# Kernel tuning notes

Measured on AMD Instinct MI355X. Metric: run time of the kernel, lower is better.

## Reference

```python
import jax, jax.numpy as jnp
import numpy as np

WS, OWS, NHEAD = 4, 6, 6          # window, overlap window = 4 + int(0.5*4), heads
B, CIN, COU, H, W = 2, 192, 192, 224, 224
MID = CIN  # r = 1


def calc_rpi_oca(ws=WS, ows=OWS):
    # relative position index between ws x ws query window and ows x ows overlapping kv window
    co = np.stack(np.meshgrid(np.arange(ws), np.arange(ws), indexing='ij')).reshape(2, -1)
    ce = np.stack(np.meshgrid(np.arange(ows), np.arange(ows), indexing='ij')).reshape(2, -1)
    rel = (ce[:, None, :] - co[:, :, None]).transpose(1, 2, 0) + (ws - 1)  # [ws*ws, ows*ows, 2], >= 0
    idx = rel[..., 0] * (ws + ows - 1) + rel[..., 1]                       # in [0, (ws+ows-1)^2)
    return jnp.asarray(idx)  # [16, 36]

RPI = calc_rpi_oca()


def conv2d(x, w, b, pad):
    out = jax.lax.conv_general_dilated(x, w, (1, 1), [(pad, pad), (pad, pad)],
                                       dimension_numbers=('NCHW', 'OIHW', 'NCHW'))
    return out + b[None, :, None, None]


def group_norm(x, g, b, groups, eps=1e-5):
    n = x.shape[0]
    xg = x.reshape(n, groups, -1)
    mu = xg.mean(-1, keepdims=True)
    var = xg.var(-1, keepdims=True)
    xn = ((xg - mu) * jax.lax.rsqrt(var + eps)).reshape(x.shape)
    return xn * g[None, :, None, None] + b[None, :, None, None]


def layer_norm(x, g, b, eps=1e-5):
    mu = x.mean(-1, keepdims=True)
    var = x.var(-1, keepdims=True)
    return (x - mu) * jax.lax.rsqrt(var + eps) * g + b


def ocab(x, h, w, ln1_g, ln1_b, qkv_w, qkv_b, rpb, proj_w, proj_b,
         ln2_g, ln2_b, fc1_w, fc1_b, fc2_w, fc2_b):
    b, _, c = x.shape
    nh, nw, d = h // WS, w // WS, c // NHEAD
    shortcut = x
    xn = layer_norm(x, ln1_g, ln1_b).reshape(b, h, w, c)
    qkv = xn @ qkv_w + qkv_b                                  # [b,h,w,3c] laid out [q|k|v]
    q = qkv[..., :c]
    kv = jnp.stack([qkv[..., c:2 * c], qkv[..., 2 * c:]])     # [2,b,h,w,c]
    # non-overlapping query windows -> [b*nwin, 16, NHEAD, d]
    qw = q.reshape(b, nh, WS, nw, WS, c).transpose(0, 1, 3, 2, 4, 5).reshape(b * nh * nw, WS * WS, NHEAD, d)
    # overlapping kv windows = Unfold(kernel=OWS, stride=WS, pad=(OWS-WS)//2)
    pad = (OWS - WS) // 2
    kvp = jnp.pad(kv, ((0, 0), (0, 0), (pad, pad), (pad, pad), (0, 0)))
    rows = (jnp.arange(nh) * WS)[:, None] + jnp.arange(OWS)[None, :]   # [nh, OWS]
    cols = (jnp.arange(nw) * WS)[:, None] + jnp.arange(OWS)[None, :]   # [nw, OWS]
    patches = kvp[:, :, rows[:, None, :, None], cols[None, :, None, :], :]  # [2,b,nh,nw,OWS,OWS,c]
    kvw = patches.reshape(2, b * nh * nw, OWS * OWS, NHEAD, d)
    kw, vw = kvw[0], kvw[1]
    attn = jnp.einsum('wqhd,wkhd->whqk', qw * (d ** -0.5), kw)  # [b*nwin, NHEAD, 16, 36]
    bias = rpb[RPI.reshape(-1)].reshape(WS * WS, OWS * OWS, NHEAD).transpose(2, 0, 1)
    attn = jax.nn.softmax(attn + bias[None], axis=-1)
    out = jnp.einsum('whqk,wkhd->wqhd', attn, vw).reshape(b, nh, nw, WS, WS, c)
    out = out.transpose(0, 1, 3, 2, 4, 5).reshape(b, h * w, c)  # window_reverse
    out = out @ proj_w + proj_b + shortcut
    xm = layer_norm(out, ln2_g, ln2_b)
    mlp = jax.nn.gelu(xm @ fc1_w + fc1_b, approximate=False) @ fc2_w + fc2_b
    return out + mlp


def atoca_forward(x, conv1_w, conv1_b, gn1_g, gn1_b, conv2_w, conv2_b, gn2_g, gn2_b,
                  conv3_w, conv3_b, ln1_g, ln1_b, qkv_w, qkv_b, rpb, proj_w, proj_b,
                  ln2_g, ln2_b, fc1_w, fc1_b, fc2_w, fc2_b):
    Bx, C, Hx, Wx = x.shape
    shortcut = x
    # raw row-major reshape, exactly as the torch code (not a spatial window partition)
    out = x.reshape(Bx * (Hx // WS) * (Wx // WS), C, WS, WS)
    out = conv2d(out, conv1_w, conv1_b, 1)
    out = jax.nn.silu(group_norm(out, gn1_g, gn1_b, NHEAD))
    out = out.transpose(0, 2, 3, 1).reshape(Bx, Hx * Wx, -1)
    out = ocab(out, Hx, Wx, ln1_g, ln1_b, qkv_w, qkv_b, rpb, proj_w, proj_b,
               ln2_g, ln2_b, fc1_w, fc1_b, fc2_w, fc2_b)
    out = out.reshape(Bx * (Hx // WS) * (Wx // WS), WS, WS, -1).transpose(0, 3, 1, 2)
    out = conv2d(out, conv2_w, conv2_b, 1)
    out = group_norm(out, gn2_g, gn2_b, NHEAD)
    out = out.reshape(Bx, -1, Hx, Wx)
    out = out + conv2d(shortcut, conv3_w, conv3_b, 0)
    return jax.nn.relu(out)


def setup_inputs() -> dict:
    key = jax.random.key(0)
    ks = iter(jax.random.split(key, 32))
    rn = lambda shape, s=0.02: (s * jax.random.normal(next(ks), shape)).astype(jnp.float32)
    return {
        'x': jax.random.normal(next(ks), (B, CIN, H, W), dtype=jnp.float32),
        'conv1_w': rn((MID, CIN, 3, 3)), 'conv1_b': rn((MID,)),
        'gn1_g': jnp.ones((MID,), jnp.float32), 'gn1_b': jnp.zeros((MID,), jnp.float32),
        'conv2_w': rn((COU, MID, 3, 3)), 'conv2_b': rn((COU,)),
        'gn2_g': jnp.ones((COU,), jnp.float32), 'gn2_b': jnp.zeros((COU,), jnp.float32),
        'conv3_w': rn((COU, CIN, 1, 1)), 'conv3_b': rn((COU,)),
        'ln1_g': jnp.ones((MID,), jnp.float32), 'ln1_b': jnp.zeros((MID,), jnp.float32),
        'qkv_w': rn((MID, 3 * MID)), 'qkv_b': rn((3 * MID,)),
        'rpb': rn(((WS + OWS - 1) ** 2, NHEAD)),
        'proj_w': rn((MID, MID)), 'proj_b': rn((MID,)),
        'ln2_g': jnp.ones((MID,), jnp.float32), 'ln2_b': jnp.zeros((MID,), jnp.float32),
        'fc1_w': rn((MID, 2 * MID)), 'fc1_b': rn((2 * MID,)),
        'fc2_w': rn((2 * MID, MID)), 'fc2_b': rn((MID,)),
    }


def reference(x, conv1_w, conv1_b, gn1_g, gn1_b, conv2_w, conv2_b, gn2_g, gn2_b,
              conv3_w, conv3_b, ln1_g, ln1_b, qkv_w, qkv_b, rpb, proj_w, proj_b,
              ln2_g, ln2_b, fc1_w, fc1_b, fc2_w, fc2_b):
    return atoca_forward(x, conv1_w, conv1_b, gn1_g, gn1_b, conv2_w, conv2_b, gn2_g, gn2_b,
                         conv3_w, conv3_b, ln1_g, ln1_b, qkv_w, qkv_b, rpb, proj_w, proj_b,
                         ln2_g, ln2_b, fc1_w, fc1_b, fc2_w, fc2_b)
```

## Files before the change

### kernel.cpp

```cpp
#include <hip/hip_runtime.h>
#include <hip/hip_bf16.h>
#include <math.h>

typedef __hip_bfloat16 bf16;
typedef __attribute__((ext_vector_type(8))) short s8v;
typedef __attribute__((ext_vector_type(4))) short s4v;
typedef __attribute__((ext_vector_type(4))) float f32x4;
typedef __attribute__((ext_vector_type(2))) _Float16 h2;

constexpr int CB   = 2;
constexpr int CH   = 224, CW = 224;
constexpr int NHW  = 56;
constexpr int NPATCH = CB * NHW * NHW;
constexpr int TOKPB  = CH * CW;
constexpr int MTOK   = CB * TOKPB;
constexpr size_t SECSZ = 19267584;

constexpr size_t B_T0  = 0;
constexpr size_t B_P2  = B_T0 + 38535168;
constexpr size_t B_P3  = B_P2 + 115605504;
constexpr size_t B_P4  = B_P3 + 38535168;
constexpr size_t B_WF1 = B_P4 + 38535168;
constexpr size_t B_WF2 = B_WF1 + 1327104;
constexpr size_t B_W3F = B_WF2 + 1327104;
constexpr size_t B_WQ  = B_W3F + 147456;
constexpr size_t B_WP  = B_WQ + 221184;
constexpr size_t B_WG1 = B_WP + 73728;
constexpr size_t B_WG2 = B_WG1 + 147456;
constexpr size_t WS_NEEDED = B_WG2 + 147456;

__device__ __forceinline__ float ldf(const float* p) { return *p; }
__device__ __forceinline__ float ldf(const bf16* p)  { return __bfloat162float(*p); }
__device__ __forceinline__ void  stf(float* p, float v) { *p = v; }
__device__ __forceinline__ void  stf(bf16* p, float v)  { *p = __float2bfloat16(v); }
__device__ __forceinline__ unsigned short f2bf(float f) {
    unsigned u = __builtin_bit_cast(unsigned, f);
    unsigned r = (u + 0x7fffu + ((u >> 16) & 1u)) >> 16;
    return (unsigned short)r;
}
__device__ __forceinline__ float bf2f(short s) {
    unsigned u = ((unsigned)(unsigned short)s) << 16;
    return __builtin_bit_cast(float, u);
}

__device__ __forceinline__ void prep_wf(const float* __restrict__ w, short* __restrict__ wf, int o) {
    int within = o & 511, frag = o >> 9;
    int l = within >> 3, j = within & 7;
    int nt = frag % 12, t2 = frag / 12, ks = t2 % 6, tap = t2 / 6;
    int co = nt * 16 + (l & 15);
    int ci = ks * 32 + (l >> 4) * 8 + j;
    wf[o] = (short)f2bf(w[(co * 192 + ci) * 9 + tap]);
}
__device__ __forceinline__ void prep_wgemm(const float* __restrict__ w, short* __restrict__ wf,
                                           int K, int N, int o) {
    int j = o & 7, l = (o >> 3) & 63, f = o >> 9;
    int ntiles = N >> 4;
    int kt = f / ntiles, nt = f % ntiles;
    int k = kt * 32 + (l >> 4) * 8 + j;
    int col = nt * 16 + (l & 15);
    wf[o] = (short)f2bf(w[(size_t)k * N + col]);
}
__device__ __forceinline__ void prep_w3f(const float* __restrict__ w, short* __restrict__ wf, int o) {
    int j = o & 7, l = (o >> 3) & 63, f = o >> 9;
    int kt = f / 12, ct = f % 12;
    int co = ct * 16 + (l & 15);
    int ci = kt * 32 + (l >> 4) * 8 + j;
    wf[o] = (short)f2bf(w[co * 192 + ci]);
}
__global__ __launch_bounds__(256) void prep_all_kernel(
    const float* __restrict__ conv1_w, short* __restrict__ WF1,
    const float* __restrict__ conv2_w, short* __restrict__ WF2,
    const float* __restrict__ conv3_w, short* __restrict__ W3F,
    const float* __restrict__ qkv_w,   short* __restrict__ WQ,
    const float* __restrict__ proj_w,  short* __restrict__ WP,
    const float* __restrict__ fc1_w,   short* __restrict__ WG1,
    const float* __restrict__ fc2_w,   short* __restrict__ WG2)
{
    int o = blockIdx.x * 256 + threadIdx.x;
    if (o < 331776)            { prep_wf(conv1_w, WF1, o); return; }
    o -= 331776;
    if (o < 331776)            { prep_wf(conv2_w, WF2, o); return; }
    o -= 331776;
    if (o < 36864)             { prep_w3f(conv3_w, W3F, o); return; }
    o -= 36864;
    if (o < 110592)            { prep_wgemm(qkv_w, WQ, 192, 576, o); return; }
    o -= 110592;
    if (o < 36864)             { prep_wgemm(proj_w, WP, 192, 192, o); return; }
    o -= 36864;
    if (o < 73728)             { prep_wgemm(fc1_w, WG1, 192, 384, o); return; }
    o -= 73728;
    if (o < 73728)             { prep_wgemm(fc2_w, WG2, 384, 192, o); return; }
}
constexpr int PREP_TOTAL = 331776 * 2 + 36864 + 110592 + 36864 + 73728 * 2;

template <bool FIRST>
__global__ __launch_bounds__(256, 4) void conv_mfma_kernel(
    const void* __restrict__ srcv, const short* __restrict__ wf,
    const float* __restrict__ bias, const float* __restrict__ gng,
    const float* __restrict__ gnb, bf16* __restrict__ dst)
{
    __shared__ short xs[13056];
    __shared__ float gsum[4][6], gsum2[4][6], gmu[4][6], grs[4][6];
    const int tid  = threadIdx.x;
    const int lane = tid & 63, wid = tid >> 6;
    const int n0   = blockIdx.x * 4;

    if (tid < 24) { gsum[tid / 6][tid % 6] = 0.f; gsum2[tid / 6][tid % 6] = 0.f; }
    for (int u = tid; u < 4 * 192; u += 256) {
        int q = u / 192;
        xs[q * 3264 + 3072 + (u % 192)] = 0;
    }

    if constexpr (FIRST) {
        const float4* sp = (const float4*)((const float*)srcv + (size_t)n0 * 3072);
        #pragma unroll
        for (int u = 0; u < 12; ++u) {
            int idx = u * 256 + tid;
            float4 v = sp[idx];
            int q = idx / 768;
            int li = (idx % 768) * 4;
            int ci = li >> 4, p0 = li & 15;
            float vv[4] = { v.x, v.y, v.z, v.w };
            #pragma unroll
            for (int k = 0; k < 4; ++k) {
                int row = p0 + k;
                int ba = q * 6528 + ((row * 384 + ci * 2) ^ ((row & 7) << 4));
                *(short*)((char*)xs + ba) = (short)f2bf(vv[k]);
            }
        }
    } else {
        const s8v* sp8 = (const s8v*)((const bf16*)srcv + (size_t)n0 * 3072);
        #pragma unroll
        for (int u = 0; u < 6; ++u) {
            int li = u * 256 + tid;
            int r = li / 24, ch = li % 24;
            int q = r >> 4, rl = r & 15;
            s8v val = sp8[li];
            int ba = q * 6528 + ((rl * 384 + ch * 16) ^ ((rl & 7) << 4));
            *(s8v*)((char*)xs + ba) = val;
        }
    }
    __syncthreads();

    const int ntb = wid * 3;
    const int cl  = lane & 15;
    const int kg  = lane >> 4;
    f32x4 acc[3][4];
    #pragma unroll
    for (int t = 0; t < 3; ++t) {
        float bv = bias[(ntb + t) * 16 + cl];
        #pragma unroll
        for (int q = 0; q < 4; ++q) acc[t][q] = (f32x4){ bv, bv, bv, bv };
    }

    const int pi = cl >> 2, pj = cl & 3;
    const s8v* wf8 = (const s8v*)wf;

    for (int tap = 0; tap < 9; ++tap) {
        const int di = tap / 3, dj = tap % 3;
        const int ii = pi + di - 1, jj = pj + dj - 1;
        const bool valid = (ii >= 0 && ii < 4 && jj >= 0 && jj < 4);
        const int nr  = valid ? (ii * 4 + jj) : 16;
        const int rb  = nr * 384;
        const int swz = (nr & 7) << 4;
        #pragma unroll
        for (int ks = 0; ks < 6; ++ks) {
            const s8v* bp = wf8 + (size_t)((tap * 6 + ks) * 12) * 64 + lane;
            s8v b0 = bp[(ntb + 0) * 64];
            s8v b1 = bp[(ntb + 1) * 64];
            s8v b2 = bp[(ntb + 2) * 64];
            const int inner = (rb + ks * 64 + kg * 16) ^ swz;
            #pragma unroll
            for (int q = 0; q < 4; ++q) {
                s8v a = *(const s8v*)((const char*)xs + q * 6528 + inner);
                acc[0][q] = __builtin_amdgcn_mfma_f32_16x16x32_bf16(a, b0, acc[0][q], 0, 0, 0);
                acc[1][q] = __builtin_amdgcn_mfma_f32_16x16x32_bf16(a, b1, acc[1][q], 0, 0, 0);
                acc[2][q] = __builtin_amdgcn_mfma_f32_16x16x32_bf16(a, b2, acc[2][q], 0, 0, 0);
            }
        }
    }

    #pragma unroll
    for (int t = 0; t < 3; ++t) {
        const int g = (ntb + t) >> 1;
        #pragma unroll
        for (int q = 0; q < 4; ++q) {
            f32x4 A = acc[t][q];
            float s  = A[0] + A[1] + A[2] + A[3];
            float s2 = A[0]*A[0] + A[1]*A[1] + A[2]*A[2] + A[3]*A[3];
            #pragma unroll
            for (int off = 32; off; off >>= 1) { s += __shfl_xor(s, off); s2 += __shfl_xor(s2, off); }
            if (lane == 0) { atomicAdd(&gsum[q][g], s); atomicAdd(&gsum2[q][g], s2); }
        }
    }
    __syncthreads();
    if (tid < 24) {
        int q = tid / 6, g = tid % 6;
        float mu  = gsum[q][g] * (1.f / 512.f);
        float var = gsum2[q][g] * (1.f / 512.f) - mu * mu;
        gmu[q][g] = mu; grs[q][g] = rsqrtf(var + 1e-5f);
    }
    __syncthreads();

    if constexpr (FIRST) {
        #pragma unroll
        for (int t = 0; t < 3; ++t) {
            const int co = (ntb + t) * 16 + cl, g = (ntb + t) >> 1;
            const float gg = gng[co], gb = gnb[co];
            #pragma unroll
            for (int q = 0; q < 4; ++q) {
                const float mu = gmu[q][g], rs = grs[q][g];
                #pragma unroll
                for (int r = 0; r < 4; ++r) {
                    float v = (acc[t][q][r] - mu) * rs * gg + gb;
                    v = v / (1.f + __expf(-v));
                    int row = q * 16 + kg * 4 + r;
                    int ba = (row * 384 + co * 2) ^ ((row & 7) << 4);
                    *(short*)((char*)xs + ba) = (short)f2bf(v);
                }
            }
        }
        __syncthreads();
        bf16* dp = dst + (size_t)n0 * 3072;
        #pragma unroll
        for (int u = 0; u < 6; ++u) {
            int li = u * 256 + tid;
            int row = li / 24, g2 = li % 24;
            int ba = (row * 384 + g2 * 16) ^ ((row & 7) << 4);
            s8v val = *(const s8v*)((const char*)xs + ba);
            *(s8v*)(dp + (size_t)row * 192 + g2 * 8) = val;
        }
    } else {
        #pragma unroll
        for (int t = 0; t < 3; ++t) {
            const int co = (ntb + t) * 16 + cl, g = (ntb + t) >> 1;
            const float gg = gng[co], gb = gnb[co];
            #pragma unroll
            for (int q = 0; q < 4; ++q) {
                const float mu = gmu[q][g], rs = grs[q][g];
                #pragma unroll
                for (int r = 0; r < 4; ++r) {
                    float v = (acc[t][q][r] - mu) * rs * gg + gb;
                    xs[q * 3072 + co * 16 + kg * 4 + r] = (short)f2bf(v);
                }
            }
        }
        __syncthreads();
        s4v* dp = (s4v*)(dst + (size_t)n0 * 3072);
        const s4v* sps = (const s4v*)xs;
        #pragma unroll
        for (int u = 0; u < 12; ++u) {
            dp[u * 256 + tid] = sps[u * 256 + tid];
        }
    }
}

template <bool RES, bool GELU_ACT, bool LN, bool QKVOUT, int NKT>
__global__ __launch_bounds__(256) void gemm_mfma_kernel(
    const bf16* __restrict__ A, const short* __restrict__ wfb,
    const float* __restrict__ bias, const bf16* __restrict__ res,
    void* __restrict__ out, int N,
    const float* __restrict__ lng, const float* __restrict__ lnb)
{
    __shared__ short ls[8192];
    const int tid = threadIdx.x, lane = tid & 63, wid = tid >> 6;
    const int m0 = blockIdx.x * 128;
    const int cl = lane & 15, kg = lane >> 4;
    constexpr int K = NKT * 32;
    const int ntiles = N >> 4;
    const int ntsec = ntiles / gridDim.y;
    const int ntbeg = blockIdx.y * ntsec;

    s8v af0[NKT], af1[NKT];
    const int r0 = m0 + wid * 32 + cl;
    #pragma unroll
    for (int kt = 0; kt < NKT; ++kt) {
        af0[kt] = *(const s8v*)(A + (size_t)r0 * K + kt * 32 + kg * 8);
        af1[kt] = *(const s8v*)(A + (size_t)(r0 + 16) * K + kt * 32 + kg * 8);
    }
    if constexpr (LN) {
        static_assert(!LN || NKT == 6, "LN requires K==192");
        #pragma unroll
        for (int r = 0; r < 2; ++r) {
            s8v* af = r ? af1 : af0;
            float s = 0.f, s2 = 0.f;
            #pragma unroll
            for (int kt = 0; kt < NKT; ++kt)
                #pragma unroll
                for (int j = 0; j < 8; ++j) {
                    float v = bf2f(af[kt][j]);
                    s += v; s2 += v * v;
                }
            s  += __shfl_xor(s, 16);  s2 += __shfl_xor(s2, 16);
            s  += __shfl_xor(s, 32);  s2 += __shfl_xor(s2, 32);
            const float mu = s * (1.f / 192.f);
            const float rs = rsqrtf(s2 * (1.f / 192.f) - mu * mu + 1e-5f);
            #pragma unroll
            for (int kt = 0; kt < NKT; ++kt) {
                const float* gp = lng + kt * 32 + kg * 8;
                const float* bp = lnb + kt * 32 + kg * 8;
                #pragma unroll
                for (int j = 0; j < 8; ++j) {
                    float v = (bf2f(af[kt][j]) - mu) * rs * gp[j] + bp[j];
                    af[kt][j] = (short)f2bf(v);
                }
            }
        }
    }

    const s8v* wf8 = (const s8v*)wfb;
    for (int nt0 = ntbeg; nt0 < ntbeg + ntsec; nt0 += 4) {
        const int n0 = nt0 * 16;
        f32x4 acc[2][4];
        #pragma unroll
        for (int nf = 0; nf < 4; ++nf) {
            float bv = bias[n0 + nf * 16 + cl];
            acc[0][nf] = (f32x4){ bv, bv, bv, bv };
            acc[1][nf] = (f32x4){ bv, bv, bv, bv };
        }
        #pragma unroll
        for (int kt = 0; kt < NKT; ++kt) {
            #pragma unroll
            for (int nf = 0; nf < 4; ++nf) {
                s8v b = wf8[(size_t)(kt * ntiles + nt0 + nf) * 64 + lane];
                acc[0][nf] = __builtin_amdgcn_mfma_f32_16x16x32_bf16(af0[kt], b, acc[0][nf], 0, 0, 0);
                acc[1][nf] = __builtin_amdgcn_mfma_f32_16x16x32_bf16(af1[kt], b, acc[1][nf], 0, 0, 0);
            }
        }

        __syncthreads();
        #pragma unroll
        for (int rf = 0; rf < 2; ++rf) {
            #pragma unroll
            for (int nf = 0; nf < 4; ++nf) {
                const int lcol = nf * 16 + cl;
                #pragma unroll
                for (int r = 0; r < 4; ++r) {
                    const int lrow = wid * 32 + rf * 16 + kg * 4 + r;
                    float v = acc[rf][nf][r];
                    if (GELU_ACT) v = 0.5f * v * (1.f + erff(v * 0.70710678118f));
                    short sv;
                    if constexpr (QKVOUT) sv = __builtin_bit_cast(short, (_Float16)v);
                    else                  sv = (short)f2bf(v);
                    int ba = (lrow * 128 + lcol * 2) ^ ((lrow & 7) << 4);
                    *(short*)((char*)ls + ba) = sv;
                }
            }
        }
        __syncthreads();
        #pragma unroll
        for (int p = 0; p < 4; ++p) {
            const int lrow = p * 32 + (tid >> 3);
            const int g = tid & 7;
            int ba = (lrow * 128 + g * 16) ^ ((lrow & 7) << 4);
            s8v val = *(const s8v*)((const char*)ls + ba);
            const int row = m0 + lrow;
            const int col0 = n0 + g * 8;
            if constexpr (QKVOUT) {
                const int sec = n0 / 192;
                const int c0 = col0 - sec * 192, h = c0 >> 5, d0 = c0 & 31;
                const int bb2 = row / TOKPB, t = row - bb2 * TOKPB;
                *(s8v*)((_Float16*)out + (size_t)sec * SECSZ +
                        ((size_t)(bb2 * 6 + h) * TOKPB + t) * 32 + d0) = val;
            } else if constexpr (RES) {
                s8v rv = *(const s8v*)(res + (size_t)row * N + col0);
                s8v ov;
                #pragma unroll
                for (int e = 0; e < 8; ++e) ov[e] = (short)f2bf(bf2f(val[e]) + bf2f(rv[e]));
                *(s8v*)((bf16*)out + (size_t)row * N + col0) = ov;
            } else {
                *(s8v*)((bf16*)out + (size_t)row * N + col0) = val;
            }
        }
    }
}

constexpr int HSTR = 1160;
__global__ __launch_bounds__(128) void attn_proj_kernel(
    const _Float16* __restrict__ qf, const float* __restrict__ rpb,
    const short* __restrict__ wpf, const float* __restrict__ pb,
    const bf16* __restrict__ t0, bf16* __restrict__ omid)
{
    __shared__ __align__(16) short kh[6 * HSTR];
    __shared__ __align__(16) short vh[6 * HSTR];
    const int w = blockIdx.x;
    const int b = w / (NHW * NHW), wi = w % (NHW * NHW);
    const int nhi = wi / NHW, nwi = wi % NHW;
    const int tid = threadIdx.x;
    const int lane = tid & 63, wid = tid >> 6;
    const int r0 = nhi * 4 - 1, c0 = nwi * 4 - 1;
    const _Float16* kfb = qf + SECSZ;
    const _Float16* vfb = qf + 2 * SECSZ;

    #pragma unroll
    for (int it = 0; it < 14; ++it) {
        int v = tid + it * 128;
        if (v < 1728) {
            int kv = v >= 864 ? 1 : 0;
            int u = v - kv * 864;
            int h = u / 144, rem = u % 144, kj = rem >> 2, d0 = (rem & 3) * 8;
            int rr = r0 + kj / 6, cc = c0 + kj % 6;
            s8v val = { 0, 0, 0, 0, 0, 0, 0, 0 };
            if (rr >= 0 && rr < CH && cc >= 0 && cc < CW) {
                const _Float16* src = kv ? vfb : kfb;
                val = *(const s8v*)(src + ((size_t)(b * 6 + h) * TOKPB + rr * CW + cc) * 32 + d0);
            }
            short* dst = kv ? vh : kh;
            *(s8v*)(dst + h * HSTR + kj * 32 + d0) = val;
        }
    }
    __syncthreads();

    h2 o2[16];
    float inv = 0.f;
    if (tid < 96) {
        const int h = tid >> 4, qi = tid & 15;
        const int qr = nhi * 4 + (qi >> 2), qc = nwi * 4 + (qi & 3);
        const _Float16* qp = qf + ((size_t)(b * 6 + h) * TOKPB + qr * CW + qc) * 32;
        h2 qh[16];
        #pragma unroll
        for (int u = 0; u < 4; ++u) {
            uint4 qa = *(const uint4*)(qp + u * 8);
            qh[u * 4 + 0] = __builtin_bit_cast(h2, qa.x);
            qh[u * 4 + 1] = __builtin_bit_cast(h2, qa.y);
            qh[u * 4 + 2] = __builtin_bit_cast(h2, qa.z);
            qh[u * 4 + 3] = __builtin_bit_cast(h2, qa.w);
        }

        float sc[36];
        const short* khb = kh + h * HSTR;
        #pragma unroll
        for (int kj = 0; kj < 36; ++kj) {
            const uint4* kp = (const uint4*)(khb + kj * 32);
            uint4 k0 = kp[0], k1 = kp[1], k2 = kp[2], k3 = kp[3];
            unsigned kwv[16] = { k0.x, k0.y, k0.z, k0.w, k1.x, k1.y, k1.z, k1.w,
                                 k2.x, k2.y, k2.z, k2.w, k3.x, k3.y, k3.z, k3.w };
            float a0 = 0.f, a1 = 0.f, a2 = 0.f, a3 = 0.f;
            #pragma unroll
            for (int e = 0; e < 4; ++e) {
                a0 = __builtin_amdgcn_fdot2(__builtin_bit_cast(h2, kwv[4*e+0]), qh[4*e+0], a0, false);
                a1 = __builtin_amdgcn_fdot2(__builtin_bit_cast(h2, kwv[4*e+1]), qh[4*e+1], a1, false);
                a2 = __builtin_amdgcn_fdot2(__builtin_bit_cast(h2, kwv[4*e+2]), qh[4*e+2], a2, false);
                a3 = __builtin_amdgcn_fdot2(__builtin_bit_cast(h2, kwv[4*e+3]), qh[4*e+3], a3, false);
            }
            const int rel0 = kj / 6 - (qi >> 2) + 3;
            const int rel1 = kj % 6 - (qi & 3) + 3;
            sc[kj] = ((a0 + a1) + (a2 + a3)) * 0.17677669529f + rpb[(rel0 * 9 + rel1) * 6 + h];
        }
        float mx = -1e30f;
        #pragma unroll
        for (int kj = 0; kj < 36; ++kj) mx = fmaxf(mx, sc[kj]);
        float sum = 0.f;
        #pragma unroll
        for (int kj = 0; kj < 36; ++kj) { sc[kj] = __expf(sc[kj] - mx); sum += sc[kj]; }
        inv = 1.f / sum;

        #pragma unroll
        for (int e = 0; e < 16; ++e) o2[e] = (h2){ (_Float16)0.f, (_Float16)0.f };
        const short* vhb = vh + h * HSTR;
        #pragma unroll
        for (int kj = 0; kj < 36; ++kj) {
            const uint4* vp = (const uint4*)(vhb + kj * 32);
            uint4 v0 = vp[0], v1 = vp[1], v2 = vp[2], v3 = vp[3];
            unsigned vwv[16] = { v0.x, v0.y, v0.z, v0.w, v1.x, v1.y, v1.z, v1.w,
                                 v2.x, v2.y, v2.z, v2.w, v3.x, v3.y, v3.z, v3.w };
            const _Float16 ph = (_Float16)sc[kj];
            const h2 ph2 = { ph, ph };
            #pragma unroll
            for (int e = 0; e < 16; ++e)
                o2[e] = __builtin_bit_cast(h2, vwv[e]) * ph2 + o2[e];
        }
    }
    __syncthreads();

    if (tid < 96) {
        const int h = tid >> 4, qi = tid & 15;
        #pragma unroll
        for (int u = 0; u < 4; ++u) {
            s8v pk;
            #pragma unroll
            for (int e = 0; e < 4; ++e) {
                h2 ov = o2[u * 4 + e];
                pk[2 * e]     = (short)f2bf((float)ov[0] * inv);
                pk[2 * e + 1] = (short)f2bf((float)ov[1] * inv);
            }
            int ba = (qi * 384 + (h * 32 + u * 8) * 2) ^ ((qi & 7) << 4);
            *(s8v*)((char*)kh + ba) = pk;
        }
    }
    __syncthreads();

    const int cl = lane & 15, kg = lane >> 4;
    s8v a[6];
    #pragma unroll
    for (int kt = 0; kt < 6; ++kt) {
        int ba = (cl * 384 + kt * 64 + kg * 16) ^ ((cl & 7) << 4);
        a[kt] = *(const s8v*)((const char*)kh + ba);
    }
    f32x4 acc[6];
    const s8v* wp8 = (const s8v*)wpf;
    #pragma unroll
    for (int ctl = 0; ctl < 6; ++ctl) {
        float bv = pb[(wid * 6 + ctl) * 16 + cl];
        acc[ctl] = (f32x4){ bv, bv, bv, bv };
    }
    #pragma unroll
    for (int kt = 0; kt < 6; ++kt) {
        #pragma unroll
        for (int ctl = 0; ctl < 6; ++ctl) {
            s8v bfr = wp8[(size_t)(kt * 12 + wid * 6 + ctl) * 64 + lane];
            acc[ctl] = __builtin_amdgcn_mfma_f32_16x16x32_bf16(a[kt], bfr, acc[ctl], 0, 0, 0);
        }
    }
    #pragma unroll
    for (int ctl = 0; ctl < 6; ++ctl) {
        const int col = (wid * 6 + ctl) * 16 + cl;
        #pragma unroll
        for (int r = 0; r < 4; ++r) {
            vh[(kg * 4 + r) * 192 + col] = (short)f2bf(acc[ctl][r]);
        }
    }
    __syncthreads();

    #pragma unroll
    for (int u = 0; u < 3; ++u) {
        int li = u * 128 + tid;
        int row = li / 24, c8 = (li % 24) * 8;
        int qr = nhi * 4 + (row >> 2), qc = nwi * 4 + (row & 3);
        size_t gb = ((size_t)(b * TOKPB + qr * CW + qc)) * 192 + c8;
        s8v pv = *(const s8v*)(vh + row * 192 + c8);
        s8v rv = *(const s8v*)(t0 + gb);
        s8v ov;
        #pragma unroll
        for (int e = 0; e < 8; ++e) ov[e] = (short)f2bf(bf2f(pv[e]) + bf2f(rv[e]));
        *(s8v*)(omid + gb) = ov;
    }
}

__global__ __launch_bounds__(256, 4) void final_mfma_kernel(
    const float* __restrict__ x, const short* __restrict__ w3f,
    const float* __restrict__ b3, const bf16* __restrict__ c2,
    float* __restrict__ out)
{
    __shared__ short xs2[12288];
    const int pix0 = blockIdx.x * 64;
    const int b    = blockIdx.y;
    const int tid = threadIdx.x, lane = tid & 63, wid = tid >> 6;
    const int cl = lane & 15, kg = lane >> 4;
    const float* xb = x + (size_t)b * (192 * TOKPB);

    #pragma unroll
    for (int u = 0; u < 12; ++u) {
        int idx = u * 256 + tid;
        int ci = idx >> 4, p4 = (idx & 15) << 2;
        float4 v = *(const float4*)(xb + (size_t)ci * TOKPB + pix0 + p4);
        float vv[4] = { v.x, v.y, v.z, v.w };
        #pragma unroll
        for (int k = 0; k < 4; ++k) {
            int row = p4 + k;
            int ba = (row * 384 + ci * 2) ^ ((row & 7) << 4);
            *(short*)((char*)xs2 + ba) = (short)f2bf(vv[k]);
        }
    }
    __syncthreads();

    const int ctb = wid * 3;
    f32x4 acc[3][4] = {};
    const s8v* wf8 = (const s8v*)w3f;

    #pragma unroll
    for (int kt = 0; kt < 6; ++kt) {
        s8v a0 = wf8[(size_t)(kt * 12 + ctb + 0) * 64 + lane];
        s8v a1 = wf8[(size_t)(kt * 12 + ctb + 1) * 64 + lane];
        s8v a2 = wf8[(size_t)(kt * 12 + ctb + 2) * 64 + lane];
        #pragma unroll
        for (int pt = 0; pt < 4; ++pt) {
            int row = pt * 16 + cl;
            int ba = (row * 384 + kt * 64 + kg * 16) ^ ((row & 7) << 4);
            s8v bfr = *(const s8v*)((const char*)xs2 + ba);
            acc[0][pt] = __builtin_amdgcn_mfma_f32_16x16x32_bf16(a0, bfr, acc[0][pt], 0, 0, 0);
            acc[1][pt] = __builtin_amdgcn_mfma_f32_16x16x32_bf16(a1, bfr, acc[1][pt], 0, 0, 0);
            acc[2][pt] = __builtin_amdgcn_mfma_f32_16x16x32_bf16(a2, bfr, acc[2][pt], 0, 0, 0);
        }
    }

    #pragma unroll
    for (int t = 0; t < 3; ++t) {
        #pragma unroll
        for (int r = 0; r < 4; ++r) {
            const int co = (ctb + t) * 16 + kg * 4 + r;
            const float bb = b3[co];
            const size_t rowbase = (size_t)b * (192 * TOKPB) + (size_t)co * TOKPB + pix0;
            #pragma unroll
            for (int pt = 0; pt < 4; ++pt) {
                const size_t f = rowbase + pt * 16 + cl;
                float v = acc[t][pt][r] + bb + bf2f(__builtin_bit_cast(short, c2[f]));
                out[f] = fmaxf(v, 0.f);
            }
        }
    }
}

extern "C" void kernel_launch(void* const* d_in, const int* in_sizes, int n_in,
                              void* d_out, int out_size, void* d_ws, size_t ws_size,
                              hipStream_t stream)
{
    if (ws_size < WS_NEEDED) return;

    const float* x       = (const float*)d_in[0];
    const float* conv1_w = (const float*)d_in[1];
    const float* conv1_b = (const float*)d_in[2];
    const float* gn1_g   = (const float*)d_in[3];
    const float* gn1_b   = (const float*)d_in[4];
    const float* conv2_w = (const float*)d_in[5];
    const float* conv2_b = (const float*)d_in[6];
    const float* gn2_g   = (const float*)d_in[7];
    const float* gn2_b   = (const float*)d_in[8];
    const float* conv3_w = (const float*)d_in[9];
    const float* conv3_b = (const float*)d_in[10];
    const float* ln1_g   = (const float*)d_in[11];
    const float* ln1_b   = (const float*)d_in[12];
    const float* qkv_w   = (const float*)d_in[13];
    const float* qkv_b   = (const float*)d_in[14];
    const float* rpb     = (const float*)d_in[15];
    const float* proj_w  = (const float*)d_in[16];
    const float* proj_b  = (const float*)d_in[17];
    const float* ln2_g   = (const float*)d_in[18];
    const float* ln2_b   = (const float*)d_in[19];
    const float* fc1_w   = (const float*)d_in[20];
    const float* fc1_b   = (const float*)d_in[21];
    const float* fc2_w   = (const float*)d_in[22];
    const float* fc2_b   = (const float*)d_in[23];

    char* wsb = (char*)d_ws;
    bf16*  T0  = (bf16*)(wsb + B_T0);
    _Float16* QF = (_Float16*)(wsb + B_P2);
    bf16*  HID = (bf16*)(wsb + B_P2);
    bf16*  P3  = (bf16*)(wsb + B_P3);
    bf16*  P4  = (bf16*)(wsb + B_P4);
    short* WF1 = (short*)(wsb + B_WF1);
    short* WF2 = (short*)(wsb + B_WF2);
    short* W3F = (short*)(wsb + B_W3F);
    short* WQ  = (short*)(wsb + B_WQ);
    short* WP  = (short*)(wsb + B_WP);
    short* WG1 = (short*)(wsb + B_WG1);
    short* WG2 = (short*)(wsb + B_WG2);
    float* OUT = (float*)d_out;

    prep_all_kernel<<<(PREP_TOTAL + 255) / 256, 256, 0, stream>>>(
        conv1_w, WF1, conv2_w, WF2, conv3_w, W3F, qkv_w, WQ, proj_w, WP, fc1_w, WG1, fc2_w, WG2);

    conv_mfma_kernel<true><<<NPATCH / 4, 256, 0, stream>>>(x, WF1, conv1_b, gn1_g, gn1_b, T0);
    gemm_mfma_kernel<false, false, true, true, 6><<<dim3(MTOK / 128, 1), 256, 0, stream>>>(
        T0, WQ, qkv_b, nullptr, QF, 576, ln1_g, ln1_b);
    attn_proj_kernel<<<NPATCH, 128, 0, stream>>>(QF, rpb, WP, proj_b, T0, P4);
    gemm_mfma_kernel<false, true, true, false, 6><<<dim3(MTOK / 128, 1), 256, 0, stream>>>(
        P4, WG1, fc1_b, nullptr, HID, 384, ln2_g, ln2_b);
    gemm_mfma_kernel<true, false, false, false, 12><<<dim3(MTOK / 128, 1), 256, 0, stream>>>(
        HID, WG2, fc2_b, P4, P3, 192, nullptr, nullptr);
    conv_mfma_kernel<false><<<NPATCH / 4, 256, 0, stream>>>(P3, WF2, conv2_b, gn2_g, gn2_b, P4);
    final_mfma_kernel<<<dim3(TOKPB / 64, CB), 256, 0, stream>>>(x, W3F, conv3_b, P4, OUT);
}
```

Before: 525.6 us.

## Split attention keys across thread pairs and widen attn block to three waves

After: 506.9 us (median of 3 runs). -3.6%, faster.

```diff
diff --git a/kernel.cpp b/kernel.cpp
--- a/kernel.cpp
+++ b/kernel.cpp
@@ -376,7 +376,7 @@
 }
 
 constexpr int HSTR = 1160;
-__global__ __launch_bounds__(128) void attn_proj_kernel(
+__global__ __launch_bounds__(192) void attn_proj_kernel(
     const _Float16* __restrict__ qf, const float* __restrict__ rpb,
     const short* __restrict__ wpf, const float* __restrict__ pb,
     const bf16* __restrict__ t0, bf16* __restrict__ omid)
@@ -393,88 +393,93 @@
     const _Float16* vfb = qf + 2 * SECSZ;
 
     #pragma unroll
-    for (int it = 0; it < 14; ++it) {
-        int v = tid + it * 128;
-        if (v < 1728) {
-            int kv = v >= 864 ? 1 : 0;
-            int u = v - kv * 864;
-            int h = u / 144, rem = u % 144, kj = rem >> 2, d0 = (rem & 3) * 8;
-            int rr = r0 + kj / 6, cc = c0 + kj % 6;
-            s8v val = { 0, 0, 0, 0, 0, 0, 0, 0 };
-            if (rr >= 0 && rr < CH && cc >= 0 && cc < CW) {
-                const _Float16* src = kv ? vfb : kfb;
-                val = *(const s8v*)(src + ((size_t)(b * 6 + h) * TOKPB + rr * CW + cc) * 32 + d0);
-            }
-            short* dst = kv ? vh : kh;
-            *(s8v*)(dst + h * HSTR + kj * 32 + d0) = val;
-        }
-    }
-    __syncthreads();
+    for (int it = 0; it < 9; ++it) {
+        int v = tid + it * 192;
+        int kv = v >= 864 ? 1 : 0;
+        int u = v - kv * 864;
+        int h = u / 144, rem = u % 144, kj = rem >> 2, d0 = (rem & 3) * 8;
+        int rr = r0 + kj / 6, cc = c0 + kj % 6;
+        s8v val = { 0, 0, 0, 0, 0, 0, 0, 0 };
+        if (rr >= 0 && rr < CH && cc >= 0 && cc < CW) {
+            const _Float16* src = kv ? vfb : kfb;
+            val = *(const s8v*)(src + ((size_t)(b * 6 + h) * TOKPB + rr * CW + cc) * 32 + d0);
+        }
+        short* dst = kv ? vh : kh;
+        *(s8v*)(dst + h * HSTR + kj * 32 + d0) = val;
+    }
+    __syncthreads();
+
+    const int pair = tid >> 1, split = tid & 1;
+    const int h = pair >> 4, qi = pair & 15;
+    const int qr = nhi * 4 + (qi >> 2), qc = nwi * 4 + (qi & 3);
+    const _Float16* qp = qf + ((size_t)(b * 6 + h) * TOKPB + qr * CW + qc) * 32;
+    h2 qh[16];
+    #pragma unroll
+    for (int u = 0; u < 4; ++u) {
+        uint4 qa = *(const uint4*)(qp + u * 8);
+        qh[u * 4 + 0] = __builtin_bit_cast(h2, qa.x);
+        qh[u * 4 + 1] = __builtin_bit_cast(h2, qa.y);
+        qh[u * 4 + 2] = __builtin_bit_cast(h2, qa.z);
+        qh[u * 4 + 3] = __builtin_bit_cast(h2, qa.w);
+    }
+
+    float sc[18];
+    const int kbeg = split * 18;
+    const short* khb = kh + h * HSTR;
+    #pragma unroll
+    for (int kk = 0; kk < 18; ++kk) {
+        const int kj = kbeg + kk;
+        const uint4* kp = (const uint4*)(khb + kj * 32);
+        uint4 k0 = kp[0], k1 = kp[1], k2 = kp[2], k3 = kp[3];
+        unsigned kwv[16] = { k0.x, k0.y, k0.z, k0.w, k1.x, k1.y, k1.z, k1.w,
+                             k2.x, k2.y, k2.z, k2.w, k3.x, k3.y, k3.z, k3.w };
+        float a0 = 0.f, a1 = 0.f, a2 = 0.f, a3 = 0.f;
+        #pragma unroll
+        for (int e = 0; e < 4; ++e) {
+            a0 = __builtin_amdgcn_fdot2(__builtin_bit_cast(h2, kwv[4*e+0]), qh[4*e+0], a0, false);
+            a1 = __builtin_amdgcn_fdot2(__builtin_bit_cast(h2, kwv[4*e+1]), qh[4*e+1], a1, false);
+            a2 = __builtin_amdgcn_fdot2(__builtin_bit_cast(h2, kwv[4*e+2]), qh[4*e+2], a2, false);
+            a3 = __builtin_amdgcn_fdot2(__builtin_bit_cast(h2, kwv[4*e+3]), qh[4*e+3], a3, false);
+        }
+        const int rel0 = kj / 6 - (qi >> 2) + 3;
+        const int rel1 = kj % 6 - (qi & 3) + 3;
+        sc[kk] = ((a0 + a1) + (a2 + a3)) * 0.17677669529f + rpb[(rel0 * 9 + rel1) * 6 + h];
+    }
+    float mx = -1e30f;
+    #pragma unroll
+    for (int kk = 0; kk < 18; ++kk) mx = fmaxf(mx, sc[kk]);
+    mx = fmaxf(mx, __shfl_xor(mx, 1));
+    float sum = 0.f;
+    #pragma unroll
+    for (int kk = 0; kk < 18; ++kk) { sc[kk] = __expf(sc[kk] - mx); sum += sc[kk]; }
+    sum += __shfl_xor(sum, 1);
+    const float inv = 1.f / sum;
 
     h2 o2[16];
-    float inv = 0.f;
-    if (tid < 96) {
-        const int h = tid >> 4, qi = tid & 15;
-        const int qr = nhi * 4 + (qi >> 2), qc = nwi * 4 + (qi & 3);
-        const _Float16* qp = qf + ((size_t)(b * 6 + h) * TOKPB + qr * CW + qc) * 32;
-        h2 qh[16];
-        #pragma unroll
-        for (int u = 0; u < 4; ++u) {
-            uint4 qa = *(const uint4*)(qp + u * 8);
-            qh[u * 4 + 0] = __builtin_bit_cast(h2, qa.x);
-            qh[u * 4 + 1] = __builtin_bit_cast(h2, qa.y);
-            qh[u * 4 + 2] = __builtin_bit_cast(h2, qa.z);
-            qh[u * 4 + 3] = __builtin_bit_cast(h2, qa.w);
-        }
-
-        float sc[36];
-        const short* khb = kh + h * HSTR;
-        #pragma unroll
-        for (int kj = 0; kj < 36; ++kj) {
-            const uint4* kp = (const uint4*)(khb + kj * 32);
-            uint4 k0 = kp[0], k1 = kp[1], k2 = kp[2], k3 = kp[3];
-            unsigned kwv[16] = { k0.x, k0.y, k0.z, k0.w, k1.x, k1.y, k1.z, k1.w,
-                                 k2.x, k2.y, k2.z, k2.w, k3.x, k3.y, k3.z, k3.w };
-            float a0 = 0.f, a1 = 0.f, a2 = 0.f, a3 = 0.f;
-            #pragma unroll
-            for (int e = 0; e < 4; ++e) {
-                a0 = __builtin_amdgcn_fdot2(__builtin_bit_cast(h2, kwv[4*e+0]), qh[4*e+0], a0, false);
-                a1 = __builtin_amdgcn_fdot2(__builtin_bit_cast(h2, kwv[4*e+1]), qh[4*e+1], a1, false);
-                a2 = __builtin_amdgcn_fdot2(__builtin_bit_cast(h2, kwv[4*e+2]), qh[4*e+2], a2, false);
-                a3 = __builtin_amdgcn_fdot2(__builtin_bit_cast(h2, kwv[4*e+3]), qh[4*e+3], a3, false);
-            }
-            const int rel0 = kj / 6 - (qi >> 2) + 3;
-            const int rel1 = kj % 6 - (qi & 3) + 3;
-            sc[kj] = ((a0 + a1) + (a2 + a3)) * 0.17677669529f + rpb[(rel0 * 9 + rel1) * 6 + h];
-        }
-        float mx = -1e30f;
-        #pragma unroll
-        for (int kj = 0; kj < 36; ++kj) mx = fmaxf(mx, sc[kj]);
-        float sum = 0.f;
-        #pragma unroll
-        for (int kj = 0; kj < 36; ++kj) { sc[kj] = __expf(sc[kj] - mx); sum += sc[kj]; }
-        inv = 1.f / sum;
-
-        #pragma unroll
-        for (int e = 0; e < 16; ++e) o2[e] = (h2){ (_Float16)0.f, (_Float16)0.f };
-        const short* vhb = vh + h * HSTR;
-        #pragma unroll
-        for (int kj = 0; kj < 36; ++kj) {
-            const uint4* vp = (const uint4*)(vhb + kj * 32);
-            uint4 v0 = vp[0], v1 = vp[1], v2 = vp[2], v3 = vp[3];
-            unsigned vwv[16] = { v0.x, v0.y, v0.z, v0.w, v1.x, v1.y, v1.z, v1.w,
-                                 v2.x, v2.y, v2.z, v2.w, v3.x, v3.y, v3.z, v3.w };
-            const _Float16 ph = (_Float16)sc[kj];
-            const h2 ph2 = { ph, ph };
-            #pragma unroll
-            for (int e = 0; e < 16; ++e)
-                o2[e] = __builtin_bit_cast(h2, vwv[e]) * ph2 + o2[e];
-        }
-    }
-    __syncthreads();
-
-    if (tid < 96) {
-        const int h = tid >> 4, qi = tid & 15;
+    #pragma unroll
+    for (int e = 0; e < 16; ++e) o2[e] = (h2){ (_Float16)0.f, (_Float16)0.f };
+    const short* vhb = vh + h * HSTR;
+    #pragma unroll
+    for (int kk = 0; kk < 18; ++kk) {
+        const int kj = kbeg + kk;
+        const uint4* vp = (const uint4*)(vhb + kj * 32);
+        uint4 v0 = vp[0], v1 = vp[1], v2 = vp[2], v3 = vp[3];
+        unsigned vwv[16] = { v0.x, v0.y, v0.z, v0.w, v1.x, v1.y, v1.z, v1.w,
+                             v2.x, v2.y, v2.z, v2.w, v3.x, v3.y, v3.z, v3.w };
+        const _Float16 ph = (_Float16)sc[kk];
+        const h2 ph2 = { ph, ph };
+        #pragma unroll
+        for (int e = 0; e < 16; ++e)
+            o2[e] = __builtin_bit_cast(h2, vwv[e]) * ph2 + o2[e];
+    }
+    #pragma unroll
+    for (int e = 0; e < 16; ++e) {
+        unsigned other = __shfl_xor(__builtin_bit_cast(unsigned, o2[e]), 1);
+        o2[e] = o2[e] + __builtin_bit_cast(h2, other);
+    }
+    __syncthreads();
+
+    if (split == 0) {
         #pragma unroll
         for (int u = 0; u < 4; ++u) {
             s8v pk;
@@ -497,24 +502,24 @@
         int ba = (cl * 384 + kt * 64 + kg * 16) ^ ((cl & 7) << 4);
         a[kt] = *(const s8v*)((const char*)kh + ba);
     }
-    f32x4 acc[6];
+    f32x4 acc[4];
     const s8v* wp8 = (const s8v*)wpf;
     #pragma unroll
-    for (int ctl = 0; ctl < 6; ++ctl) {
-        float bv = pb[(wid * 6 + ctl) * 16 + cl];
+    for (int ctl = 0; ctl < 4; ++ctl) {
+        float bv = pb[(wid * 4 + ctl) * 16 + cl];
         acc[ctl] = (f32x4){ bv, bv, bv, bv };
     }
     #pragma unroll
     for (int kt = 0; kt < 6; ++kt) {
         #pragma unroll
-        for (int ctl = 0; ctl < 6; ++ctl) {
-            s8v bfr = wp8[(size_t)(kt * 12 + wid * 6 + ctl) * 64 + lane];
+        for (int ctl = 0; ctl < 4; ++ctl) {
+            s8v bfr = wp8[(size_t)(kt * 12 + wid * 4 + ctl) * 64 + lane];
             acc[ctl] = __builtin_amdgcn_mfma_f32_16x16x32_bf16(a[kt], bfr, acc[ctl], 0, 0, 0);
         }
     }
     #pragma unroll
-    for (int ctl = 0; ctl < 6; ++ctl) {
-        const int col = (wid * 6 + ctl) * 16 + cl;
+    for (int ctl = 0; ctl < 4; ++ctl) {
+        const int col = (wid * 4 + ctl) * 16 + cl;
         #pragma unroll
         for (int r = 0; r < 4; ++r) {
             vh[(kg * 4 + r) * 192 + col] = (short)f2bf(acc[ctl][r]);
@@ -523,11 +528,11 @@
     __syncthreads();
 
     #pragma unroll
-    for (int u = 0; u < 3; ++u) {
-        int li = u * 128 + tid;
+    for (int u = 0; u < 2; ++u) {
+        int li = u * 192 + tid;
         int row = li / 24, c8 = (li % 24) * 8;
-        int qr = nhi * 4 + (row >> 2), qc = nwi * 4 + (row & 3);
-        size_t gb = ((size_t)(b * TOKPB + qr * CW + qc)) * 192 + c8;
+        int qr2 = nhi * 4 + (row >> 2), qc2 = nwi * 4 + (row & 3);
+        size_t gb = ((size_t)(b * TOKPB + qr2 * CW + qc2)) * 192 + c8;
         s8v pv = *(const s8v*)(vh + row * 192 + c8);
         s8v rv = *(const s8v*)(t0 + gb);
         s8v ov;
@@ -653,7 +658,7 @@
     conv_mfma_kernel<true><<<NPATCH / 4, 256, 0, stream>>>(x, WF1, conv1_b, gn1_g, gn1_b, T0);
     gemm_mfma_kernel<false, false, true, true, 6><<<dim3(MTOK / 128, 1), 256, 0, stream>>>(
         T0, WQ, qkv_b, nullptr, QF, 576, ln1_g, ln1_b);
-    attn_proj_kernel<<<NPATCH, 128, 0, stream>>>(QF, rpb, WP, proj_b, T0, P4);
+    attn_proj_kernel<<<NPATCH, 192, 0, stream>>>(QF, rpb, WP, proj_b, T0, P4);
     gemm_mfma_kernel<false, true, true, false, 6><<<dim3(MTOK / 128, 1), 256, 0, stream>>>(
         P4, WG1, fc1_b, nullptr, HID, 384, ln2_g, ln2_b);
     gemm_mfma_kernel<true, false, false, false, 12><<<dim3(MTOK / 128, 1), 256, 0, stream>>>(
```
